# Kernel tuning notes

Measured on AMD Instinct MI355X. Metric: run time of the kernel, lower is better.

Reference implementation:

```python
import jax, jax.numpy as jnp
import numpy as np

TOP_K = 2


def setup_inputs() -> dict:
    key = jax.random.key(0)
    k1, k2, k3, k4 = jax.random.split(key, 4)
    B, S, D, H, E = 2, 2048, 1024, 4096, 8
    x = jax.random.normal(k1, (B, S, D), dtype=jnp.float32)
    router_w = jax.random.normal(k2, (E, D), dtype=jnp.float32) * 0.01  # nn.Linear(d, E).weight
    # kaiming-ish scaling for FFN weights
    w1 = jax.random.normal(k3, (E, H, D), dtype=jnp.float32) * (2.0 / D) ** 0.5
    b1 = jnp.zeros((E, H), dtype=jnp.float32)
    w2 = jax.random.normal(k4, (E, D, H), dtype=jnp.float32) * (2.0 / H) ** 0.5
    b2 = jnp.zeros((E, D), dtype=jnp.float32)
    return {"x": x, "router_w": router_w, "w1": w1, "b1": b1, "w2": w2, "b2": b2}


def reference(x, router_w, w1, b1, w2, b2):
    B, S, D = x.shape
    E = w1.shape[0]
    T = B * S
    x_flat = x.reshape(T, D)

    # Router: logits -> softmax -> top-k -> renormalize (eval mode: no jitter)
    logits = jnp.einsum('td,ed->te', x_flat, router_w)
    probs = jax.nn.softmax(logits, axis=-1)
    topw, topi = jax.lax.top_k(probs, TOP_K)                 # [T, k]
    topw = topw / jnp.sum(topw, axis=-1, keepdims=True)

    # Per-token combine weight for each expert: cw[t, e] = sum_k topw[t,k] * (topi[t,k]==e)
    cw = jnp.zeros((T, E), dtype=x.dtype)
    cw = cw.at[jnp.arange(T)[:, None], topi].add(topw)       # [T, E]

    # Expert FFNs (exact-erf GELU like torch F.gelu); combine weighted outputs.
    out = jnp.zeros((T, w2.shape[1]), dtype=x.dtype)
    for e in range(E):
        h = jax.nn.gelu(x_flat @ w1[e].T + b1[e], approximate=False)
        o = h @ w2[e].T + b2[e]
        out = out + cw[:, e:e + 1] * o
    return out.reshape(B, S, -1)
```

## Files before the change

kernel.cpp:

```cpp
#include <hip/hip_runtime.h>
#include <stdint.h>

typedef __attribute__((ext_vector_type(8))) short short8;
typedef __attribute__((ext_vector_type(4))) float floatx4;

#define T_TOK 4096
#define D_DIM 1024
#define H_DIM 4096
#define E_NUM 8
#define MAX_TILES 72
#define PLANE (8192ULL * 1024ULL)

static __device__ __forceinline__ ushort f2bf(float f) {
    uint32_t u = __float_as_uint(f);
    u += 0x7FFF + ((u >> 16) & 1);
    return (ushort)(u >> 16);
}

static __device__ __forceinline__ uint4 pack8(float4 a, float4 b) {
    union { ushort u[8]; uint4 v; } r;
    r.u[0] = f2bf(a.x); r.u[1] = f2bf(a.y); r.u[2] = f2bf(a.z); r.u[3] = f2bf(a.w);
    r.u[4] = f2bf(b.x); r.u[5] = f2bf(b.y); r.u[6] = f2bf(b.z); r.u[7] = f2bf(b.w);
    return r.v;
}

static __device__ __forceinline__ void gl_lds16(const void* g, void* l) {
    __builtin_amdgcn_global_load_lds(
        (const __attribute__((address_space(1))) uint32_t*)g,
        (__attribute__((address_space(3))) uint32_t*)l, 16, 0, 0);
}

__global__ __launch_bounds__(256) void cvt_all_kernel(
    const float* __restrict__ x,  ushort* __restrict__ xbf,
    const float* __restrict__ w1, ushort* __restrict__ w1bf,
    const float* __restrict__ w2, ushort* __restrict__ w2bf)
{
    const size_t NX = (size_t)T_TOK * D_DIM;
    const size_t NW = (size_t)E_NUM * H_DIM * D_DIM;
    size_t i = ((size_t)blockIdx.x * 256 + threadIdx.x) * 8;
    const float* src; ushort* dst; size_t j;
    if (i < NX)           { src = x;  dst = xbf;  j = i; }
    else if (i < NX + NW) { src = w1; dst = w1bf; j = i - NX; }
    else                  { src = w2; dst = w2bf; j = i - NX - NW; }
    float4 a = *(const float4*)(src + j);
    float4 b = *(const float4*)(src + j + 4);
    *(uint4*)(dst + j) = pack8(a, b);
}

__global__ __launch_bounds__(256) void router_kernel(
    const float* __restrict__ x, const float* __restrict__ rw,
    int* __restrict__ counts, int* __restrict__ topi, float* __restrict__ topw)
{
    __shared__ float rwS[E_NUM * D_DIM];
    int tid = threadIdx.x;
    for (int i = tid; i < E_NUM * D_DIM / 4; i += 256)
        ((float4*)rwS)[i] = ((const float4*)rw)[i];
    __syncthreads();

    int wave = tid >> 6, lane = tid & 63;
    int t = blockIdx.x * 4 + wave;
    const float* xr = x + (size_t)t * D_DIM;

    float acc[E_NUM];
#pragma unroll
    for (int e = 0; e < E_NUM; e++) acc[e] = 0.f;

    float xv[16];
#pragma unroll
    for (int j = 0; j < 4; j++)
        *(float4*)&xv[j * 4] = ((const float4*)xr)[lane * 4 + j];
#pragma unroll
    for (int j = 0; j < 16; j++) {
        int idx = lane * 16 + j;
#pragma unroll
        for (int e = 0; e < E_NUM; e++)
            acc[e] += xv[j] * rwS[e * D_DIM + idx];
    }
#pragma unroll
    for (int e = 0; e < E_NUM; e++)
        for (int off = 32; off > 0; off >>= 1)
            acc[e] += __shfl_xor(acc[e], off, 64);

    if (lane == 0) {
        float mx = acc[0];
        for (int e = 1; e < E_NUM; e++) mx = fmaxf(mx, acc[e]);
        float p[E_NUM];
        for (int e = 0; e < E_NUM; e++) p[e] = expf(acc[e] - mx);
        int i0 = 0;
        for (int e = 1; e < E_NUM; e++) if (p[e] > p[i0]) i0 = e;
        int i1 = (i0 == 0) ? 1 : 0;
        for (int e = 0; e < E_NUM; e++) if (e != i0 && p[e] > p[i1]) i1 = e;
        float w0 = p[i0], w1 = p[i1], sw = w0 + w1;
        w0 /= sw; w1 /= sw;
        topi[t * 2] = i0; topi[t * 2 + 1] = i1;
        topw[t * 2] = w0; topw[t * 2 + 1] = w1;
        atomicAdd(&counts[i0], 1);
        atomicAdd(&counts[i1], 1);
    }
}

__global__ void offsets_tiles_kernel(const int* __restrict__ counts,
                                     int* __restrict__ offsets, int* __restrict__ cursors,
                                     int* __restrict__ tile_e, int* __restrict__ tile_m0)
{
    if (threadIdx.x == 0 && blockIdx.x == 0) {
        int off = 0, n = 0;
        for (int e = 0; e < E_NUM; e++) {
            offsets[e] = off; cursors[e] = off; off += counts[e];
            for (int m0 = 0; m0 < counts[e]; m0 += 128) {
                tile_e[n] = e; tile_m0[n] = m0; n++;
            }
        }
        for (; n < MAX_TILES; n++) tile_e[n] = -1;
    }
}

__global__ __launch_bounds__(256) void assign_kernel(
    const int* __restrict__ topi, const float* __restrict__ topw,
    int* __restrict__ cursors, int* __restrict__ pair_token, float* __restrict__ pair_w,
    int* __restrict__ ppos)
{
    int t = blockIdx.x * 256 + threadIdx.x;
    if (t >= T_TOK) return;
    for (int k = 0; k < 2; k++) {
        int e = topi[t * 2 + k];
        int pos = atomicAdd(&cursors[e], 1);
        pair_token[pos] = t;
        pair_w[pos] = topw[t * 2 + k];
        ppos[t * 2 + k] = pos;
    }
}

__global__ __launch_bounds__(256) void ffn1_kernel(
    const ushort* __restrict__ xbf, const ushort* __restrict__ w1bf,
    const float* __restrict__ bias1,
    const int* __restrict__ counts, const int* __restrict__ offsets,
    const int* __restrict__ tile_e, const int* __restrict__ tile_m0,
    const int* __restrict__ pair_token, ushort* __restrict__ h)
{
    const int id = blockIdx.x;
    const int g = id >> 8;
    const int rem = id & 255;
    const int mt = g * 8 + (rem & 7);
    const int nt = rem >> 3;
    int e = tile_e[mt];
    if (e < 0) return;
    int m0 = tile_m0[mt];
    int cnt = counts[e];
    int off = offsets[e];
    int n0 = nt * 128;

    __shared__ ushort As[128 * 64];
    __shared__ ushort Bs[128 * 64];

    const int t = threadIdx.x;
    const int wave = t >> 6, lane = t & 63;
    const int wm = (wave >> 1) * 64, wn = (wave & 1) * 64;
    const int quad = lane >> 4, l16 = lane & 15;

    const int rsub = lane >> 3;
    const int cpos = lane & 7;
    const int srcElem = (cpos ^ rsub) * 8;

    const ushort* aP[4];
    const ushort* bP[4];
#pragma unroll
    for (int j = 0; j < 4; j++) {
        int row = j * 32 + wave * 8 + rsub;
        int gr = m0 + row; if (gr >= cnt) gr = cnt - 1;
        aP[j] = xbf + (size_t)pair_token[off + gr] * D_DIM + srcElem;
        bP[j] = w1bf + ((size_t)e * H_DIM + n0 + row) * D_DIM + srcElem;
    }
    char* AsB = (char*)As;
    char* BsB = (char*)Bs;
    int seg[4];
#pragma unroll
    for (int j = 0; j < 4; j++) seg[j] = j * 4096 + wave * 1024;

    int rowA[4], rowB[4];
#pragma unroll
    for (int i = 0; i < 4; i++) {
        rowA[i] = (wm + i * 16 + l16) * 128;
        rowB[i] = (wn + i * 16 + l16) * 128;
    }
    const int x7 = l16 & 7;

    floatx4 acc[4][4] = {};

    for (int k0 = 0; k0 < D_DIM; k0 += 64) {
        __syncthreads();
#pragma unroll
        for (int j = 0; j < 4; j++) gl_lds16(aP[j], AsB + seg[j]);
#pragma unroll
        for (int j = 0; j < 4; j++) gl_lds16(bP[j], BsB + seg[j]);
#pragma unroll
        for (int j = 0; j < 4; j++) { aP[j] += 64; bP[j] += 64; }
        __syncthreads();

#pragma unroll
        for (int kk = 0; kk < 2; kk++) {
            const int co = ((((kk << 2) | quad)) ^ x7) << 4;
            short8 av[4], bv[4];
#pragma unroll
            for (int i = 0; i < 4; i++) av[i] = *(const short8*)(AsB + rowA[i] + co);
#pragma unroll
            for (int i = 0; i < 4; i++) bv[i] = *(const short8*)(BsB + rowB[i] + co);
#pragma unroll
            for (int mi = 0; mi < 4; mi++)
#pragma unroll
                for (int ni = 0; ni < 4; ni++)
                    acc[mi][ni] = __builtin_amdgcn_mfma_f32_16x16x32_bf16(av[mi], bv[ni], acc[mi][ni], 0, 0, 0);
        }
    }

    float bb[4];
#pragma unroll
    for (int ni = 0; ni < 4; ni++) bb[ni] = bias1[e * H_DIM + n0 + wn + ni * 16 + l16];

#pragma unroll
    for (int mi = 0; mi < 4; mi++) {
#pragma unroll
        for (int reg = 0; reg < 4; reg++) {
            int gm = m0 + wm + mi * 16 + quad * 4 + reg;
            if (gm < cnt) {
                ushort* hrow = h + (size_t)(off + gm) * H_DIM + n0 + wn;
#pragma unroll
                for (int ni = 0; ni < 4; ni++) {
                    float v = acc[mi][ni][reg] + bb[ni];
                    v = 0.5f * v * (1.f + erff(v * 0.70710678118654752f));
                    hrow[ni * 16 + l16] = f2bf(v);
                }
            }
        }
    }
}

__global__ __launch_bounds__(256) void ffn2_kernel(
    const ushort* __restrict__ h, const ushort* __restrict__ w2bf,
    const float* __restrict__ bias2,
    const int* __restrict__ counts, const int* __restrict__ offsets,
    const int* __restrict__ tile_e, const int* __restrict__ tile_m0,
    const float* __restrict__ pair_w, float* __restrict__ o_part)
{
    const int id = blockIdx.x;
    const int g = id >> 7;
    const int rem = id & 127;
    const int mt = g * 8 + (rem & 7);
    const int ntk = rem >> 3;
    const int nt = ntk & 7;
    const int kc = ntk >> 3;
    int e = tile_e[mt];
    if (e < 0) return;
    int m0 = tile_m0[mt];
    int cnt = counts[e];
    int off = offsets[e];
    int n0 = nt * 128;
    const size_t kbase = (size_t)kc * (H_DIM / 2);

    __shared__ ushort As[128 * 64];
    __shared__ ushort Bs[128 * 64];

    const int t = threadIdx.x;
    const int wave = t >> 6, lane = t & 63;
    const int wm = (wave >> 1) * 64, wn = (wave & 1) * 64;
    const int quad = lane >> 4, l16 = lane & 15;

    const int rsub = lane >> 3;
    const int cpos = lane & 7;
    const int srcElem = (cpos ^ rsub) * 8;

    const ushort* aP[4];
    const ushort* bP[4];
#pragma unroll
    for (int j = 0; j < 4; j++) {
        int row = j * 32 + wave * 8 + rsub;
        int gr = m0 + row; if (gr >= cnt) gr = cnt - 1;
        aP[j] = h + (size_t)(off + gr) * H_DIM + kbase + srcElem;
        bP[j] = w2bf + ((size_t)e * D_DIM + n0 + row) * H_DIM + kbase + srcElem;
    }
    char* AsB = (char*)As;
    char* BsB = (char*)Bs;
    int seg[4];
#pragma unroll
    for (int j = 0; j < 4; j++) seg[j] = j * 4096 + wave * 1024;

    int rowA[4], rowB[4];
#pragma unroll
    for (int i = 0; i < 4; i++) {
        rowA[i] = (wm + i * 16 + l16) * 128;
        rowB[i] = (wn + i * 16 + l16) * 128;
    }
    const int x7 = l16 & 7;

    floatx4 acc[4][4] = {};

    for (int k0 = 0; k0 < H_DIM / 2; k0 += 64) {
        __syncthreads();
#pragma unroll
        for (int j = 0; j < 4; j++) gl_lds16(aP[j], AsB + seg[j]);
#pragma unroll
        for (int j = 0; j < 4; j++) gl_lds16(bP[j], BsB + seg[j]);
#pragma unroll
        for (int j = 0; j < 4; j++) { aP[j] += 64; bP[j] += 64; }
        __syncthreads();

#pragma unroll
        for (int kk = 0; kk < 2; kk++) {
            const int co = ((((kk << 2) | quad)) ^ x7) << 4;
            short8 av[4], bv[4];
#pragma unroll
            for (int i = 0; i < 4; i++) av[i] = *(const short8*)(AsB + rowA[i] + co);
#pragma unroll
            for (int i = 0; i < 4; i++) bv[i] = *(const short8*)(BsB + rowB[i] + co);
#pragma unroll
            for (int mi = 0; mi < 4; mi++)
#pragma unroll
                for (int ni = 0; ni < 4; ni++)
                    acc[mi][ni] = __builtin_amdgcn_mfma_f32_16x16x32_bf16(av[mi], bv[ni], acc[mi][ni], 0, 0, 0);
        }
    }

    float bb[4];
#pragma unroll
    for (int ni = 0; ni < 4; ni++)
        bb[ni] = (kc == 0) ? bias2[e * D_DIM + n0 + wn + ni * 16 + l16] : 0.f;

    float* plane = o_part + (size_t)kc * PLANE;
#pragma unroll
    for (int mi = 0; mi < 4; mi++) {
#pragma unroll
        for (int reg = 0; reg < 4; reg++) {
            int gm = m0 + wm + mi * 16 + quad * 4 + reg;
            if (gm < cnt) {
                float wgt = pair_w[off + gm];
                float* orow = plane + (size_t)(off + gm) * D_DIM + n0 + wn;
#pragma unroll
                for (int ni = 0; ni < 4; ni++)
                    orow[ni * 16 + l16] = (acc[mi][ni][reg] + bb[ni]) * wgt;
            }
        }
    }
}

__global__ __launch_bounds__(256) void combine_kernel(
    const float* __restrict__ o_part, const int* __restrict__ ppos,
    float* __restrict__ out)
{
    int t = blockIdx.x;
    int d = threadIdx.x * 4;
    size_t p0 = (size_t)ppos[t * 2] * D_DIM + d;
    size_t p1 = (size_t)ppos[t * 2 + 1] * D_DIM + d;
    float4 a = *(const float4*)(o_part + p0);
    float4 b = *(const float4*)(o_part + p1);
    float4 c = *(const float4*)(o_part + PLANE + p0);
    float4 e = *(const float4*)(o_part + PLANE + p1);
    float4 r;
    r.x = a.x + b.x + c.x + e.x;
    r.y = a.y + b.y + c.y + e.y;
    r.z = a.z + b.z + c.z + e.z;
    r.w = a.w + b.w + c.w + e.w;
    *(float4*)(out + (size_t)t * D_DIM + d) = r;
}

extern "C" void kernel_launch(void* const* d_in, const int* in_sizes, int n_in,
                              void* d_out, int out_size, void* d_ws, size_t ws_size,
                              hipStream_t stream)
{
    const float* x  = (const float*)d_in[0];
    const float* rw = (const float*)d_in[1];
    const float* w1 = (const float*)d_in[2];
    const float* b1 = (const float*)d_in[3];
    const float* w2 = (const float*)d_in[4];
    const float* b2 = (const float*)d_in[5];
    float* out = (float*)d_out;

    char* ws = (char*)d_ws;
    int*   counts     = (int*)(ws + 0);
    int*   cursors    = (int*)(ws + 256);
    int*   offsets    = (int*)(ws + 512);
    int*   tile_e     = (int*)(ws + 1024);
    int*   tile_m0    = (int*)(ws + 1536);
    int*   topi       = (int*)(ws + 2048);
    float* topw       = (float*)(ws + 34816);
    int*   pair_token = (int*)(ws + 67584);
    float* pair_w     = (float*)(ws + 100352);
    int*   ppos       = (int*)(ws + 133120);
    ushort* xbf  = (ushort*)(ws + 165888);
    ushort* w1bf = (ushort*)(ws + 8554496ULL);
    ushort* w2bf = (ushort*)(ws + 75663360ULL);
    ushort* h    = (ushort*)(ws + 142772224ULL);
    float* o_part = (float*)(ws + 8554496ULL);

    hipMemsetAsync(counts, 0, 32, stream);

    const size_t NTOT = (size_t)T_TOK * D_DIM + 2ULL * E_NUM * H_DIM * D_DIM;
    cvt_all_kernel<<<NTOT / 2048, 256, 0, stream>>>(x, xbf, w1, w1bf, w2, w2bf);

    router_kernel<<<T_TOK / 4, 256, 0, stream>>>(x, rw, counts, topi, topw);
    offsets_tiles_kernel<<<1, 64, 0, stream>>>(counts, offsets, cursors, tile_e, tile_m0);
    assign_kernel<<<T_TOK / 256, 256, 0, stream>>>(topi, topw, cursors, pair_token, pair_w, ppos);

    ffn1_kernel<<<MAX_TILES * 32, 256, 0, stream>>>(xbf, w1bf, b1, counts, offsets, tile_e, tile_m0, pair_token, h);

    ffn2_kernel<<<MAX_TILES * 16, 256, 0, stream>>>(h, w2bf, b2, counts, offsets, tile_e, tile_m0, pair_w, o_part);

    combine_kernel<<<T_TOK, 256, 0, stream>>>(o_part, ppos, out);
}
```

Before: 744.9 us.

## Double-buffer LDS tiles in both expert GEMM kernels to overlap loads with MFMA

Both grouped-GEMM kernels now keep two LDS buffers for the A and B tiles. They prefetch the next K-slice with global-to-LDS loads while running MFMAs on the current slice, which also cuts the barriers per iteration from two to one. This is meant to hide global-load latency behind compute. The cost is that LDS use per block doubles to 64 KB, which can lower the number of blocks resident per CU.

Result: slower. 814.7 us (+9.4%).

```diff
diff --git a/kernel.cpp b/kernel.cpp
--- a/kernel.cpp
+++ b/kernel.cpp
@@ -150,8 +150,8 @@
     int off = offsets[e];
     int n0 = nt * 128;
 
-    __shared__ ushort As[128 * 64];
-    __shared__ ushort Bs[128 * 64];
+    __shared__ ushort As[2][128 * 64];
+    __shared__ ushort Bs[2][128 * 64];
 
     const int t = threadIdx.x;
     const int wave = t >> 6, lane = t & 63;
@@ -171,8 +171,6 @@
         aP[j] = xbf + (size_t)pair_token[off + gr] * D_DIM + srcElem;
         bP[j] = w1bf + ((size_t)e * H_DIM + n0 + row) * D_DIM + srcElem;
     }
-    char* AsB = (char*)As;
-    char* BsB = (char*)Bs;
     int seg[4];
 #pragma unroll
     for (int j = 0; j < 4; j++) seg[j] = j * 4096 + wave * 1024;
@@ -187,16 +185,28 @@
 
     floatx4 acc[4][4] = {};
 
-    for (int k0 = 0; k0 < D_DIM; k0 += 64) {
+#pragma unroll
+    for (int j = 0; j < 4; j++) gl_lds16(aP[j], (char*)As[0] + seg[j]);
+#pragma unroll
+    for (int j = 0; j < 4; j++) gl_lds16(bP[j], (char*)Bs[0] + seg[j]);
+#pragma unroll
+    for (int j = 0; j < 4; j++) { aP[j] += 64; bP[j] += 64; }
+
+    const int NIT = D_DIM / 64;
+    for (int it = 0; it < NIT; it++) {
+        const int cur = it & 1;
         __syncthreads();
-#pragma unroll
-        for (int j = 0; j < 4; j++) gl_lds16(aP[j], AsB + seg[j]);
-#pragma unroll
-        for (int j = 0; j < 4; j++) gl_lds16(bP[j], BsB + seg[j]);
-#pragma unroll
-        for (int j = 0; j < 4; j++) { aP[j] += 64; bP[j] += 64; }
-        __syncthreads();
-
+        if (it + 1 < NIT) {
+            const int nxt = cur ^ 1;
+#pragma unroll
+            for (int j = 0; j < 4; j++) gl_lds16(aP[j], (char*)As[nxt] + seg[j]);
+#pragma unroll
+            for (int j = 0; j < 4; j++) gl_lds16(bP[j], (char*)Bs[nxt] + seg[j]);
+#pragma unroll
+            for (int j = 0; j < 4; j++) { aP[j] += 64; bP[j] += 64; }
+        }
+        const char* AsB = (const char*)As[cur];
+        const char* BsB = (const char*)Bs[cur];
 #pragma unroll
         for (int kk = 0; kk < 2; kk++) {
             const int co = ((((kk << 2) | quad)) ^ x7) << 4;
@@ -257,8 +267,8 @@
     int n0 = nt * 128;
     const size_t kbase = (size_t)kc * (H_DIM / 2);
 
-    __shared__ ushort As[128 * 64];
-    __shared__ ushort Bs[128 * 64];
+    __shared__ ushort As[2][128 * 64];
+    __shared__ ushort Bs[2][128 * 64];
 
     const int t = threadIdx.x;
     const int wave = t >> 6, lane = t & 63;
@@ -278,8 +288,6 @@
         aP[j] = h + (size_t)(off + gr) * H_DIM + kbase + srcElem;
         bP[j] = w2bf + ((size_t)e * D_DIM + n0 + row) * H_DIM + kbase + srcElem;
     }
-    char* AsB = (char*)As;
-    char* BsB = (char*)Bs;
     int seg[4];
 #pragma unroll
     for (int j = 0; j < 4; j++) seg[j] = j * 4096 + wave * 1024;
@@ -294,16 +302,28 @@
 
     floatx4 acc[4][4] = {};
 
-    for (int k0 = 0; k0 < H_DIM / 2; k0 += 64) {
+#pragma unroll
+    for (int j = 0; j < 4; j++) gl_lds16(aP[j], (char*)As[0] + seg[j]);
+#pragma unroll
+    for (int j = 0; j < 4; j++) gl_lds16(bP[j], (char*)Bs[0] + seg[j]);
+#pragma unroll
+    for (int j = 0; j < 4; j++) { aP[j] += 64; bP[j] += 64; }
+
+    const int NIT = (H_DIM / 2) / 64;
+    for (int it = 0; it < NIT; it++) {
+        const int cur = it & 1;
         __syncthreads();
-#pragma unroll
-        for (int j = 0; j < 4; j++) gl_lds16(aP[j], AsB + seg[j]);
-#pragma unroll
-        for (int j = 0; j < 4; j++) gl_lds16(bP[j], BsB + seg[j]);
-#pragma unroll
-        for (int j = 0; j < 4; j++) { aP[j] += 64; bP[j] += 64; }
-        __syncthreads();
-
+        if (it + 1 < NIT) {
+            const int nxt = cur ^ 1;
+#pragma unroll
+            for (int j = 0; j < 4; j++) gl_lds16(aP[j], (char*)As[nxt] + seg[j]);
+#pragma unroll
+            for (int j = 0; j < 4; j++) gl_lds16(bP[j], (char*)Bs[nxt] + seg[j]);
+#pragma unroll
+            for (int j = 0; j < 4; j++) { aP[j] += 64; bP[j] += 64; }
+        }
+        const char* AsB = (const char*)As[cur];
+        const char* BsB = (const char*)Bs[cur];
 #pragma unroll
         for (int kk = 0; kk < 2; kk++) {
             const int co = ((((kk << 2) | quad)) ^ x7) << 4;
```
